# Kernel tuning notes

Measured on AMD Instinct MI355X. Metric: run time of the kernel, lower is better.

## Reference

```python
import jax, jax.numpy as jnp
import numpy as np

B, R, N, F = 8, 8, 1024, 256


def setup_inputs() -> dict:
    key = jax.random.key(0)
    k1, k2 = jax.random.split(key)
    inputs = jax.random.normal(k1, (B, R, N, F), dtype=jnp.float32)
    Bs = jax.random.normal(k2, (R, F, F), dtype=jnp.float32) * 0.05
    return {"inputs": inputs, "Bs": Bs}


def reference(inputs, Bs):
    # E_r @ B_r : [B,R,N,F] x [R,F,F] -> [B,R,N,F]
    e = jnp.einsum("brnf,rfg->brng", inputs, Bs)
    # (E_r B_r) @ E_r^T : [B,R,N,F] x [B,R,M,F] -> [B,R,N,M]
    scores = jnp.einsum("brng,brmg->brnm", e, inputs)
    return jax.nn.sigmoid(scores)
```

## Files before the change

kernel.cpp:

```cpp
#include <hip/hip_runtime.h>


typedef float    f32x4 __attribute__((ext_vector_type(4)));
typedef _Float16 f16x8 __attribute__((ext_vector_type(8)));
typedef _Float16 f16x4 __attribute__((ext_vector_type(4)));

#define WS_E_OFF   0
#define WS_BST_OFF 16777216
#define WS_e_OFF   17301504

__global__ __launch_bounds__(256) void bl_convert(
    const float* __restrict__ E, const float* __restrict__ Bs,
    _Float16* __restrict__ wsE, _Float16* __restrict__ wsBsT) {
  int bid = blockIdx.x, tid = threadIdx.x;
  if (bid < 8192) {
    int cid = (bid << 8) + tid;
    int br  = cid >> 15;
    int rem = cid & 32767;
    int fc  = rem >> 10;
    int n   = rem & 1023;
    const float* src = E + ((size_t)br << 18) + n * 256 + (fc << 3);
    f32x4 v0 = *(const f32x4*)src;
    f32x4 v1 = *(const f32x4*)(src + 4);
    f16x8 h;
    h[0] = (_Float16)v0[0]; h[1] = (_Float16)v0[1];
    h[2] = (_Float16)v0[2]; h[3] = (_Float16)v0[3];
    h[4] = (_Float16)v1[0]; h[5] = (_Float16)v1[1];
    h[6] = (_Float16)v1[2]; h[7] = (_Float16)v1[3];
    *(f16x8*)(wsE + ((size_t)br << 18) + (fc << 13) + (n << 3)) = h;
  } else {
    int cid = ((bid - 8192) << 8) + tid;
    int r   = cid >> 13;
    int rem = cid & 8191;
    int fc  = rem >> 8;
    int g   = rem & 255;
    const float* src = Bs + (r << 16) + (fc << 3) * 256 + g;
    f16x8 h;
#pragma unroll
    for (int j = 0; j < 8; ++j) h[j] = (_Float16)src[j * 256];
    *(f16x8*)(wsBsT + (r << 16) + (fc << 11) + (g << 3)) = h;
  }
}

__global__ __launch_bounds__(256) void bl_gemm1(
    const _Float16* __restrict__ wsE, const _Float16* __restrict__ wsBsT,
    _Float16* __restrict__ wse) {
  __shared__ _Float16 sA[8192];
  __shared__ _Float16 sB[8192];
  int b0  = blockIdx.x;
  int bid = ((b0 & 7) << 7) + (b0 >> 3);
  int br = bid >> 4;
  int t  = bid & 15;
  int n0 = (t >> 1) << 7;
  int g0 = (t & 1) << 7;
  int r  = br & 7;
  int tid  = threadIdx.x;
  int lane = tid & 63, wave = tid >> 6;
  int wm = wave >> 1, wn = wave & 1;
  int quad = lane >> 4, l16 = lane & 15;

  const _Float16* aG = wsE   + ((size_t)br << 18) + (n0 << 3);
  const _Float16* bG = wsBsT + (r << 16) + (g0 << 3);

  f32x4 acc[4][4] = {};

  for (int kk = 0; kk < 4; ++kk) {
    f16x8 va[4], vb[4];
#pragma unroll
    for (int i = 0; i < 4; ++i) {
      int c = (i << 8) + tid;
      int kcl = c >> 7, nl = c & 127;
      va[i] = *(const f16x8*)(aG + (((kk << 3) + kcl) << 13) + (nl << 3));
    }
#pragma unroll
    for (int i = 0; i < 4; ++i) {
      int c = (i << 8) + tid;
      int kcl = c >> 7, gl = c & 127;
      vb[i] = *(const f16x8*)(bG + (((kk << 3) + kcl) << 11) + (gl << 3));
    }
    __syncthreads();
#pragma unroll
    for (int i = 0; i < 4; ++i) {
      int c = (i << 8) + tid;
      *(f16x8*)&sA[c << 3] = va[i];
      *(f16x8*)&sB[c << 3] = vb[i];
    }
    __syncthreads();
#pragma unroll
    for (int ks = 0; ks < 2; ++ks) {
      int kc = (ks << 2) + quad;
      f16x8 af[4], bf[4];
#pragma unroll
      for (int rt = 0; rt < 4; ++rt)
        af[rt] = *(const f16x8*)&sA[((kc << 7) + (wm << 6) + (rt << 4) + l16) << 3];
#pragma unroll
      for (int ct = 0; ct < 4; ++ct)
        bf[ct] = *(const f16x8*)&sB[((kc << 7) + (wn << 6) + (ct << 4) + l16) << 3];
#pragma unroll
      for (int rt = 0; rt < 4; ++rt)
#pragma unroll
        for (int ct = 0; ct < 4; ++ct)
          acc[rt][ct] = __builtin_amdgcn_mfma_f32_16x16x32_f16(bf[ct], af[rt], acc[rt][ct], 0, 0, 0);
    }
  }
  _Float16* eB = wse + ((size_t)br << 18);
#pragma unroll
  for (int rt = 0; rt < 4; ++rt) {
    int n = n0 + (wm << 6) + (rt << 4) + l16;
#pragma unroll
    for (int ct = 0; ct < 4; ++ct) {
      int g  = g0 + (wn << 6) + (ct << 4) + (quad << 2);
      int gc = g >> 3, gj = g & 7;
      f16x4 h;
#pragma unroll
      for (int i = 0; i < 4; ++i) h[i] = (_Float16)acc[rt][ct][i];
      *(f16x4*)(eB + (gc << 13) + (n << 3) + gj) = h;
    }
  }
}

__global__ __launch_bounds__(256) void bl_gemm2(
    const _Float16* __restrict__ wse, const _Float16* __restrict__ wsE,
    float* __restrict__ out) {
  __shared__ _Float16 sA[8192];
  __shared__ _Float16 sB[8192];
  int b0  = blockIdx.x;
  int bid = ((b0 & 7) << 9) + (b0 >> 3);
  int br = bid >> 6;
  int t  = bid & 63;
  int n0 = (t >> 3) << 7;
  int m0 = (t & 7) << 7;
  int tid  = threadIdx.x;
  int lane = tid & 63, wave = tid >> 6;
  int wm = wave >> 1, wn = wave & 1;
  int quad = lane >> 4, l16 = lane & 15;

  const _Float16* aG = wse + ((size_t)br << 18) + (n0 << 3);
  const _Float16* bG = wsE + ((size_t)br << 18) + (m0 << 3);

  f32x4 acc[4][4] = {};

  for (int kk = 0; kk < 4; ++kk) {
    f16x8 va[4], vb[4];
#pragma unroll
    for (int i = 0; i < 4; ++i) {
      int c = (i << 8) + tid;
      int kcl = c >> 7, nl = c & 127;
      va[i] = *(const f16x8*)(aG + (((kk << 3) + kcl) << 13) + (nl << 3));
    }
#pragma unroll
    for (int i = 0; i < 4; ++i) {
      int c = (i << 8) + tid;
      int kcl = c >> 7, ml = c & 127;
      vb[i] = *(const f16x8*)(bG + (((kk << 3) + kcl) << 13) + (ml << 3));
    }
    __syncthreads();
#pragma unroll
    for (int i = 0; i < 4; ++i) {
      int c = (i << 8) + tid;
      *(f16x8*)&sA[c << 3] = va[i];
      *(f16x8*)&sB[c << 3] = vb[i];
    }
    __syncthreads();
#pragma unroll
    for (int ks = 0; ks < 2; ++ks) {
      int kc = (ks << 2) + quad;
      f16x8 af[4], bf[4];
#pragma unroll
      for (int rt = 0; rt < 4; ++rt)
        af[rt] = *(const f16x8*)&sA[((kc << 7) + (wm << 6) + (rt << 4) + l16) << 3];
#pragma unroll
      for (int ct = 0; ct < 4; ++ct)
        bf[ct] = *(const f16x8*)&sB[((kc << 7) + (wn << 6) + (ct << 4) + l16) << 3];
#pragma unroll
      for (int rt = 0; rt < 4; ++rt)
#pragma unroll
        for (int ct = 0; ct < 4; ++ct)
          acc[rt][ct] = __builtin_amdgcn_mfma_f32_16x16x32_f16(bf[ct], af[rt], acc[rt][ct], 0, 0, 0);
    }
  }
  float* oB = out + ((size_t)br << 20);
#pragma unroll
  for (int rt = 0; rt < 4; ++rt) {
    int n = n0 + (wm << 6) + (rt << 4) + l16;
#pragma unroll
    for (int ct = 0; ct < 4; ++ct) {
      int m = m0 + (wn << 6) + (ct << 4) + (quad << 2);
      f32x4 v;
#pragma unroll
      for (int i = 0; i < 4; ++i) {
        float x = acc[rt][ct][i];
        v[i] = __builtin_amdgcn_rcpf(1.0f + __expf(-x));
      }
      *(f32x4*)(oB + ((size_t)n << 10) + m) = v;
    }
  }
}

extern "C" void kernel_launch(void* const* d_in, const int* in_sizes, int n_in,
                              void* d_out, int out_size, void* d_ws, size_t ws_size,
                              hipStream_t stream) {
  const float* E  = (const float*)d_in[0];
  const float* Bs = (const float*)d_in[1];
  _Float16* wsE   = (_Float16*)d_ws + WS_E_OFF;
  _Float16* wsBsT = (_Float16*)d_ws + WS_BST_OFF;
  _Float16* wse   = (_Float16*)d_ws + WS_e_OFF;
  float* out = (float*)d_out;

  bl_convert<<<8448, 256, 0, stream>>>(E, Bs, wsE, wsBsT);
  bl_gemm1<<<1024, 256, 0, stream>>>(wsE, wsBsT, wse);
  bl_gemm2<<<4096, 256, 0, stream>>>(wse, wsE, out);
}
```

Baseline: 366.2 us.

## Fuse both GEMMs into one kernel keeping intermediate e tile in LDS

```diff
diff --git a/kernel.cpp b/kernel.cpp
--- a/kernel.cpp
+++ b/kernel.cpp
@@ -7,7 +7,6 @@
 
 #define WS_E_OFF   0
 #define WS_BST_OFF 16777216
-#define WS_e_OFF   17301504
 
 __global__ __launch_bounds__(256) void bl_convert(
     const float* __restrict__ E, const float* __restrict__ Bs,
@@ -42,48 +41,52 @@
   }
 }
 
-__global__ __launch_bounds__(256) void bl_gemm1(
+__global__ __launch_bounds__(512, 2) void bl_fused(
     const _Float16* __restrict__ wsE, const _Float16* __restrict__ wsBsT,
-    _Float16* __restrict__ wse) {
-  __shared__ _Float16 sA[8192];
-  __shared__ _Float16 sB[8192];
+    float* __restrict__ out) {
+  __shared__ _Float16 se[32768];
+  __shared__ _Float16 stg[32768];
   int b0  = blockIdx.x;
-  int bid = ((b0 & 7) << 7) + (b0 >> 3);
-  int br = bid >> 4;
-  int t  = bid & 15;
-  int n0 = (t >> 1) << 7;
-  int g0 = (t & 1) << 7;
-  int r  = br & 7;
-  int tid  = threadIdx.x;
+  int bid = ((b0 & 7) << 6) + (b0 >> 3);
+  int br  = bid >> 3;
+  int nb  = bid & 7;
+  int n0  = nb << 7;
+  int r   = br & 7;
+  int tid = threadIdx.x;
   int lane = tid & 63, wave = tid >> 6;
-  int wm = wave >> 1, wn = wave & 1;
   int quad = lane >> 4, l16 = lane & 15;
-
-  const _Float16* aG = wsE   + ((size_t)br << 18) + (n0 << 3);
-  const _Float16* bG = wsBsT + (r << 16) + (g0 << 3);
+  int wg  = wave >> 1;
+  int wnn = wave & 1;
+
+  const _Float16* eG  = wsE + ((size_t)br << 18);
+  const _Float16* bsG = wsBsT + (r << 16);
 
   f32x4 acc[4][4] = {};
 
   for (int kk = 0; kk < 4; ++kk) {
-    f16x8 va[4], vb[4];
+    f16x8 va[2], vb[4];
+#pragma unroll
+    for (int i = 0; i < 2; ++i) {
+      int c = (i << 9) + tid;
+      int kcl = c >> 7, nl = c & 127;
+      va[i] = *(const f16x8*)(eG + (((kk << 3) + kcl) << 13) + ((n0 + nl) << 3));
+    }
 #pragma unroll
     for (int i = 0; i < 4; ++i) {
-      int c = (i << 8) + tid;
-      int kcl = c >> 7, nl = c & 127;
-      va[i] = *(const f16x8*)(aG + (((kk << 3) + kcl) << 13) + (nl << 3));
+      int c = (i << 9) + tid;
+      int kcl = c >> 8, gl = c & 255;
+      vb[i] = *(const f16x8*)(bsG + (((kk << 3) + kcl) << 11) + (gl << 3));
+    }
+    __syncthreads();
+#pragma unroll
+    for (int i = 0; i < 2; ++i) {
+      int c = (i << 9) + tid;
+      *(f16x8*)&stg[c << 3] = va[i];
     }
 #pragma unroll
     for (int i = 0; i < 4; ++i) {
-      int c = (i << 8) + tid;
-      int kcl = c >> 7, gl = c & 127;
-      vb[i] = *(const f16x8*)(bG + (((kk << 3) + kcl) << 11) + (gl << 3));
-    }
-    __syncthreads();
-#pragma unroll
-    for (int i = 0; i < 4; ++i) {
-      int c = (i << 8) + tid;
-      *(f16x8*)&sA[c << 3] = va[i];
-      *(f16x8*)&sB[c << 3] = vb[i];
+      int c = (i << 9) + tid;
+      *(f16x8*)&stg[8192 + (c << 3)] = vb[i];
     }
     __syncthreads();
 #pragma unroll
@@ -92,10 +95,10 @@
       f16x8 af[4], bf[4];
 #pragma unroll
       for (int rt = 0; rt < 4; ++rt)
-        af[rt] = *(const f16x8*)&sA[((kc << 7) + (wm << 6) + (rt << 4) + l16) << 3];
+        af[rt] = *(const f16x8*)&stg[((kc << 7) + (wnn << 6) + (rt << 4) + l16) << 3];
 #pragma unroll
       for (int ct = 0; ct < 4; ++ct)
-        bf[ct] = *(const f16x8*)&sB[((kc << 7) + (wn << 6) + (ct << 4) + l16) << 3];
+        bf[ct] = *(const f16x8*)&stg[8192 + (((kc << 8) + (wg << 6) + (ct << 4) + l16) << 3)];
 #pragma unroll
       for (int rt = 0; rt < 4; ++rt)
 #pragma unroll
@@ -103,97 +106,89 @@
           acc[rt][ct] = __builtin_amdgcn_mfma_f32_16x16x32_f16(bf[ct], af[rt], acc[rt][ct], 0, 0, 0);
     }
   }
-  _Float16* eB = wse + ((size_t)br << 18);
 #pragma unroll
   for (int rt = 0; rt < 4; ++rt) {
-    int n = n0 + (wm << 6) + (rt << 4) + l16;
+    int n = (wnn << 6) + (rt << 4) + l16;
 #pragma unroll
     for (int ct = 0; ct < 4; ++ct) {
-      int g  = g0 + (wn << 6) + (ct << 4) + (quad << 2);
+      int g  = (wg << 6) + (ct << 4) + (quad << 2);
       int gc = g >> 3, gj = g & 7;
       f16x4 h;
 #pragma unroll
       for (int i = 0; i < 4; ++i) h[i] = (_Float16)acc[rt][ct][i];
-      *(f16x4*)(eB + (gc << 13) + (n << 3) + gj) = h;
-    }
-  }
-}
-
-__global__ __launch_bounds__(256) void bl_gemm2(
-    const _Float16* __restrict__ wse, const _Float16* __restrict__ wsE,
-    float* __restrict__ out) {
-  __shared__ _Float16 sA[8192];
-  __shared__ _Float16 sB[8192];
-  int b0  = blockIdx.x;
-  int bid = ((b0 & 7) << 9) + (b0 >> 3);
-  int br = bid >> 6;
-  int t  = bid & 63;
-  int n0 = (t >> 3) << 7;
-  int m0 = (t & 7) << 7;
-  int tid  = threadIdx.x;
-  int lane = tid & 63, wave = tid >> 6;
-  int wm = wave >> 1, wn = wave & 1;
-  int quad = lane >> 4, l16 = lane & 15;
-
-  const _Float16* aG = wse + ((size_t)br << 18) + (n0 << 3);
-  const _Float16* bG = wsE + ((size_t)br << 18) + (m0 << 3);
-
-  f32x4 acc[4][4] = {};
-
-  for (int kk = 0; kk < 4; ++kk) {
-    f16x8 va[4], vb[4];
+      *(f16x4*)&se[(gc << 10) + (n << 3) + gj] = h;
+    }
+  }
+
+  f16x8 vs[4];
+#pragma unroll
+  for (int i = 0; i < 4; ++i) {
+    int c = (i << 9) + tid;
+    int kcl = c >> 8, ml = c & 255;
+    vs[i] = *(const f16x8*)(eG + (kcl << 13) + (ml << 3));
+  }
+#pragma unroll
+  for (int rt = 0; rt < 4; ++rt)
+#pragma unroll
+    for (int ct = 0; ct < 4; ++ct) acc[rt][ct] = (f32x4){0.f, 0.f, 0.f, 0.f};
+  __syncthreads();
+
+  float* oB = out + ((size_t)br << 20);
+  int buf = 0;
+  for (int jj = 0; jj < 16; ++jj) {
+    int kk = jj & 3;
 #pragma unroll
     for (int i = 0; i < 4; ++i) {
-      int c = (i << 8) + tid;
-      int kcl = c >> 7, nl = c & 127;
-      va[i] = *(const f16x8*)(aG + (((kk << 3) + kcl) << 13) + (nl << 3));
-    }
-#pragma unroll
-    for (int i = 0; i < 4; ++i) {
-      int c = (i << 8) + tid;
-      int kcl = c >> 7, ml = c & 127;
-      vb[i] = *(const f16x8*)(bG + (((kk << 3) + kcl) << 13) + (ml << 3));
+      int c = (i << 9) + tid;
+      *(f16x8*)&stg[(buf << 14) + (c << 3)] = vs[i];
     }
     __syncthreads();
-#pragma unroll
-    for (int i = 0; i < 4; ++i) {
-      int c = (i << 8) + tid;
-      *(f16x8*)&sA[c << 3] = va[i];
-      *(f16x8*)&sB[c << 3] = vb[i];
-    }
-    __syncthreads();
+    if (jj < 15) {
+      int j2 = jj + 1;
+      int mt2 = j2 >> 2, kk2 = j2 & 3;
+#pragma unroll
+      for (int i = 0; i < 4; ++i) {
+        int c = (i << 9) + tid;
+        int kcl = c >> 8, ml = c & 255;
+        vs[i] = *(const f16x8*)(eG + (((kk2 << 3) + kcl) << 13) + (((mt2 << 8) + ml) << 3));
+      }
+    }
 #pragma unroll
     for (int ks = 0; ks < 2; ++ks) {
       int kc = (ks << 2) + quad;
       f16x8 af[4], bf[4];
 #pragma unroll
       for (int rt = 0; rt < 4; ++rt)
-        af[rt] = *(const f16x8*)&sA[((kc << 7) + (wm << 6) + (rt << 4) + l16) << 3];
+        af[rt] = *(const f16x8*)&se[((((kk << 3) + kc) << 7) + (wnn << 6) + (rt << 4) + l16) << 3];
 #pragma unroll
       for (int ct = 0; ct < 4; ++ct)
-        bf[ct] = *(const f16x8*)&sB[((kc << 7) + (wn << 6) + (ct << 4) + l16) << 3];
+        bf[ct] = *(const f16x8*)&stg[(buf << 14) + (((kc << 8) + (wg << 6) + (ct << 4) + l16) << 3)];
 #pragma unroll
       for (int rt = 0; rt < 4; ++rt)
 #pragma unroll
         for (int ct = 0; ct < 4; ++ct)
           acc[rt][ct] = __builtin_amdgcn_mfma_f32_16x16x32_f16(bf[ct], af[rt], acc[rt][ct], 0, 0, 0);
     }
-  }
-  float* oB = out + ((size_t)br << 20);
-#pragma unroll
-  for (int rt = 0; rt < 4; ++rt) {
-    int n = n0 + (wm << 6) + (rt << 4) + l16;
-#pragma unroll
-    for (int ct = 0; ct < 4; ++ct) {
-      int m = m0 + (wn << 6) + (ct << 4) + (quad << 2);
-      f32x4 v;
-#pragma unroll
-      for (int i = 0; i < 4; ++i) {
-        float x = acc[rt][ct][i];
-        v[i] = __builtin_amdgcn_rcpf(1.0f + __expf(-x));
+    if (kk == 3) {
+      int mt = jj >> 2;
+#pragma unroll
+      for (int rt = 0; rt < 4; ++rt) {
+        int n = n0 + (wnn << 6) + (rt << 4) + l16;
+#pragma unroll
+        for (int ct = 0; ct < 4; ++ct) {
+          int m = (mt << 8) + (wg << 6) + (ct << 4) + (quad << 2);
+          f32x4 v;
+#pragma unroll
+          for (int i = 0; i < 4; ++i) {
+            float x = acc[rt][ct][i];
+            v[i] = __builtin_amdgcn_rcpf(1.0f + __expf(-x));
+          }
+          *(f32x4*)(oB + ((size_t)n << 10) + m) = v;
+          acc[rt][ct] = (f32x4){0.f, 0.f, 0.f, 0.f};
+        }
       }
-      *(f32x4*)(oB + ((size_t)n << 10) + m) = v;
-    }
+    }
+    buf ^= 1;
   }
 }
 
@@ -204,10 +199,8 @@
   const float* Bs = (const float*)d_in[1];
   _Float16* wsE   = (_Float16*)d_ws + WS_E_OFF;
   _Float16* wsBsT = (_Float16*)d_ws + WS_BST_OFF;
-  _Float16* wse   = (_Float16*)d_ws + WS_e_OFF;
   float* out = (float*)d_out;
 
   bl_convert<<<8448, 256, 0, stream>>>(E, Bs, wsE, wsBsT);
-  bl_gemm1<<<1024, 256, 0, stream>>>(wsE, wsBsT, wse);
-  bl_gemm2<<<4096, 256, 0, stream>>>(wse, wsE, out);
+  bl_fused<<<512, 512, 0, stream>>>(wsE, wsBsT, out);
 }
```

Result: slower. 378.4 us (+3.3%).
